# Performance work log

Measured on AMD Instinct MI355X. Metric: run time of the kernel, lower is better.

Reference implementation:

```python
import jax, jax.numpy as jnp
import numpy as np

FG_FRACTION = 0.5
BATCHSIZE = 256
NUM_IMAGES = 1
NUM_CLASSES = 21
FG_THRESH = 0.5
BG_THRESH_HI = 0.5
BG_THRESH_LO = 0.1
ROIS_PER_IMAGE = BATCHSIZE // NUM_IMAGES                      # 256
FG_ROIS_PER_IMAGE = int(round(FG_FRACTION * ROIS_PER_IMAGE))  # 128
BG_ROIS_PER_IMAGE = ROIS_PER_IMAGE - FG_ROIS_PER_IMAGE        # 128


def _make_boxes(key, n, img=1000.0, max_wh=200.0):
    k1, k2 = jax.random.split(key)
    xy = jax.random.uniform(k1, (n, 2), dtype=jnp.float32) * (img - max_wh)
    wh = jax.random.uniform(k2, (n, 2), dtype=jnp.float32) * max_wh + 1.0
    return jnp.concatenate([xy, xy + wh], axis=1)  # valid [x1,y1,x2,y2]


def setup_inputs() -> dict:
    key = jax.random.key(0)
    k1, k2, k3 = jax.random.split(key, 3)
    N, G = 250000, 128
    rois = _make_boxes(k1, N)
    all_rois = jnp.concatenate([jnp.zeros((N, 1), jnp.float32), rois], axis=1)  # [N,5], col0 = image idx
    gt_boxes = _make_boxes(k2, G)                                               # [G,4]
    gt_labels = jax.random.randint(k3, (G,), 1, NUM_CLASSES).astype(jnp.int32)  # fg classes 1..20
    return {"all_rois": all_rois, "gt_boxes": gt_boxes, "gt_labels": gt_labels}


def _iou(a, b):
    area_a = (a[:, 2] - a[:, 0] + 1.0) * (a[:, 3] - a[:, 1] + 1.0)
    area_b = (b[:, 2] - b[:, 0] + 1.0) * (b[:, 3] - b[:, 1] + 1.0)
    ix1 = jnp.maximum(a[:, None, 0], b[None, :, 0])
    iy1 = jnp.maximum(a[:, None, 1], b[None, :, 1])
    ix2 = jnp.minimum(a[:, None, 2], b[None, :, 2])
    iy2 = jnp.minimum(a[:, None, 3], b[None, :, 3])
    iw = jnp.clip(ix2 - ix1 + 1.0, 0.0)
    ih = jnp.clip(iy2 - iy1 + 1.0, 0.0)
    inter = iw * ih
    return inter / (area_a[:, None] + area_b[None, :] - inter)


def _bbox_transform(ex, gt):
    ew = ex[:, 2] - ex[:, 0] + 1.0
    eh = ex[:, 3] - ex[:, 1] + 1.0
    ecx = ex[:, 0] + 0.5 * ew
    ecy = ex[:, 1] + 0.5 * eh
    gw = gt[:, 2] - gt[:, 0] + 1.0
    gh = gt[:, 3] - gt[:, 1] + 1.0
    gcx = gt[:, 0] + 0.5 * gw
    gcy = gt[:, 1] + 0.5 * gh
    return jnp.stack([(gcx - ecx) / ew, (gcy - ecy) / eh,
                      jnp.log(gw / ew), jnp.log(gh / eh)], axis=1)


def _proposal_target(all_rois, gt_boxes, gt_labels):
    G = gt_boxes.shape[0]
    # append gt boxes (with image-index 0 column) to the proposal set
    gt_rois = jnp.concatenate([jnp.zeros((G, 1), all_rois.dtype), gt_boxes], axis=1)
    all_rois = jnp.concatenate([all_rois, gt_rois], axis=0)          # [N+G, 5]

    overlaps = _iou(all_rois[:, 1:5], gt_boxes)                       # [N+G, G] -- dominant memory traffic
    gt_assignment = jnp.argmax(overlaps, axis=1)                      # [N+G]
    max_ov = jnp.max(overlaps, axis=1)                                # [N+G]
    labels_all = gt_labels[gt_assignment]                             # [N+G]

    fg_mask = max_ov >= FG_THRESH
    bg_mask = (max_ov < BG_THRESH_HI) & (max_ov >= BG_THRESH_LO)

    # random fg/bg sampling: top-k over random keys restricted to each mask
    u = jax.random.uniform(jax.random.key(42), (all_rois.shape[0],), dtype=jnp.float32)
    fg_idx = jax.lax.top_k(jnp.where(fg_mask, u, -1.0), FG_ROIS_PER_IMAGE)[1]
    bg_idx = jax.lax.top_k(jnp.where(bg_mask, u, -1.0), BG_ROIS_PER_IMAGE)[1]
    keep = jnp.concatenate([fg_idx, bg_idx])                          # [256]

    valid_fg = fg_mask[fg_idx]  # if fewer fg than requested, pad slots get label 0
    labels = jnp.concatenate([jnp.where(valid_fg, labels_all[fg_idx], 0),
                              jnp.zeros((BG_ROIS_PER_IMAGE,), labels_all.dtype)])

    rois = all_rois[keep]                                             # [256, 5]
    targets = _bbox_transform(rois[:, 1:5], gt_boxes[gt_assignment[keep]])  # [256, 4]

    # scatter targets into class-specific columns [256, 4*num_classes]
    onehot = jax.nn.one_hot(labels, NUM_CLASSES, dtype=targets.dtype)
    bbox_targets = (onehot[:, :, None] * targets[:, None, :]).reshape(ROIS_PER_IMAGE, 4 * NUM_CLASSES)
    bbox_targets = bbox_targets * (labels > 0)[:, None].astype(targets.dtype)
    return rois, labels, bbox_targets


def reference(all_rois, gt_boxes, gt_labels):
    return _proposal_target(all_rois, gt_boxes, gt_labels)
```

## Files before the change

### kernel.cpp

```cpp
#include <hip/hip_runtime.h>
#include <stdint.h>

#define GMAX 128
#define TK 128
#define NBINS 4096
#define CAND_MAX 4096
#define NUM_CLASSES 21

__device__ __forceinline__ void threefry2x32(uint32_t k0, uint32_t k1,
                                             uint32_t& x0, uint32_t& x1) {
  uint32_t ks0 = k0, ks1 = k1, ks2 = k0 ^ k1 ^ 0x1BD11BDAu;
  x0 += ks0; x1 += ks1;
#define TF_ROUND(r) { x0 += x1; x1 = (x1 << (r)) | (x1 >> (32 - (r))); x1 ^= x0; }
  TF_ROUND(13) TF_ROUND(15) TF_ROUND(26) TF_ROUND(6)
  x0 += ks1; x1 += ks2 + 1u;
  TF_ROUND(17) TF_ROUND(29) TF_ROUND(16) TF_ROUND(24)
  x0 += ks2; x1 += ks0 + 2u;
  TF_ROUND(13) TF_ROUND(15) TF_ROUND(26) TF_ROUND(6)
  x0 += ks0; x1 += ks1 + 3u;
  TF_ROUND(17) TF_ROUND(29) TF_ROUND(16) TF_ROUND(24)
  x0 += ks1; x1 += ks2 + 4u;
  TF_ROUND(13) TF_ROUND(15) TF_ROUND(26) TF_ROUND(6)
  x0 += ks2; x1 += ks0 + 5u;
#undef TF_ROUND
}

__global__ void __launch_bounds__(1024)
init_kernel(uint32_t* __restrict__ hist, int* __restrict__ meta) {
  int i = blockIdx.x * 1024 + threadIdx.x;
  if (i < 2 * NBINS) hist[i] = 0u;
  if (i < 4) meta[i] = 0;
}

__global__ void __launch_bounds__(256)
score_kernel(const float* __restrict__ all_rois,
             const float* __restrict__ gt_boxes,
             uint32_t* __restrict__ score,
             uint32_t* __restrict__ hist,
             int N, int M, int G) {
  __shared__ float sgx1[GMAX], sgy1[GMAX], sgx2[GMAX], sgy2[GMAX], sga[GMAX];
  const int t = threadIdx.x;
  if (t < G) {
    float x1 = gt_boxes[t * 4 + 0];
    float y1 = gt_boxes[t * 4 + 1];
    float x2 = gt_boxes[t * 4 + 2];
    float y2 = gt_boxes[t * 4 + 3];
    sgx1[t] = x1; sgy1[t] = y1; sgx2[t] = x2; sgy2[t] = y2;
    sga[t] = __fmul_rn(__fadd_rn(__fsub_rn(x2, x1), 1.0f),
                       __fadd_rn(__fsub_rn(y2, y1), 1.0f));
  }
  __syncthreads();
  const int i = blockIdx.x * 256 + t;
  if (i >= M) return;

  float bx1, by1, bx2, by2;
  if (i < N) {
    bx1 = all_rois[(size_t)i * 5 + 1];
    by1 = all_rois[(size_t)i * 5 + 2];
    bx2 = all_rois[(size_t)i * 5 + 3];
    by2 = all_rois[(size_t)i * 5 + 4];
  } else {
    int g = i - N;
    bx1 = sgx1[g]; by1 = sgy1[g]; bx2 = sgx2[g]; by2 = sgy2[g];
  }
  const float area = __fmul_rn(__fadd_rn(__fsub_rn(bx2, bx1), 1.0f),
                               __fadd_rn(__fsub_rn(by2, by1), 1.0f));
  float best = -1.0f;
  int bi = 0;
  for (int g = 0; g < G; ++g) {
    float ix1 = fmaxf(bx1, sgx1[g]);
    float iy1 = fmaxf(by1, sgy1[g]);
    float ix2 = fminf(bx2, sgx2[g]);
    float iy2 = fminf(by2, sgy2[g]);
    float iw = fmaxf(__fadd_rn(__fsub_rn(ix2, ix1), 1.0f), 0.0f);
    float ih = fmaxf(__fadd_rn(__fsub_rn(iy2, iy1), 1.0f), 0.0f);
    float inter = __fmul_rn(iw, ih);
    float uni = __fsub_rn(__fadd_rn(area, sga[g]), inter);
    float ov = __fdiv_rn(inter, uni);
    if (ov > best) { best = ov; bi = g; }
  }

  uint32_t cx0 = 0u, cx1 = (uint32_t)i;
  threefry2x32(0u, 42u, cx0, cx1);
  uint32_t ubits = (cx0 ^ cx1) >> 9;

  uint32_t fg = (best >= 0.5f) ? 1u : 0u;
  uint32_t bg = (!fg && best >= 0.1f) ? 1u : 0u;
  score[i] = (ubits << 9) | ((uint32_t)bi << 2) | (fg << 1) | bg;
  if (fg)      atomicAdd(&hist[ubits >> 11], 1u);
  else if (bg) atomicAdd(&hist[NBINS + (ubits >> 11)], 1u);
}

__global__ void __launch_bounds__(1024)
threshold_kernel(const uint32_t* __restrict__ hist, int* __restrict__ meta) {
  __shared__ uint32_t gs[1024];
  __shared__ int s_jstar;
  const int t = threadIdx.x;
  for (int m = 0; m < 2; ++m) {
    const uint32_t* h = hist + m * NBINS;
    if (t == 0) s_jstar = -1;
    __syncthreads();
    gs[t] = h[4 * t] + h[4 * t + 1] + h[4 * t + 2] + h[4 * t + 3];
    __syncthreads();
    for (int d = 1; d < 1024; d <<= 1) {
      uint32_t add = (t + d < 1024) ? gs[t + d] : 0u;
      __syncthreads();
      gs[t] += add;
      __syncthreads();
    }
    if (gs[t] >= (uint32_t)TK && (t == 1023 || gs[t + 1] < (uint32_t)TK))
      s_jstar = t;
    __syncthreads();
    if (t == 0) {
      int B = -1;
      if (s_jstar >= 0) {
        int j = s_jstar;
        uint32_t base = (j < 1023) ? gs[j + 1] : 0u;
        B = 4 * j;
        for (int b = 4 * j + 3; b >= 4 * j; --b) {
          base += h[b];
          if (base >= (uint32_t)TK) { B = b; break; }
        }
      }
      meta[m] = B;
    }
    __syncthreads();
  }
}

__global__ void __launch_bounds__(1024)
compact_kernel(const uint32_t* __restrict__ score, int M,
               const int* __restrict__ meta_bth, int* __restrict__ meta_cnt,
               uint64_t* __restrict__ cand) {
  const int i = blockIdx.x * 1024 + threadIdx.x;
  if (i >= M) return;
  uint32_t s = score[i];
  uint32_t mb = s & 3u;
  if (!mb) return;
  const int m = (mb & 2u) ? 0 : 1;
  const int Bth = meta_bth[m];
  if (Bth >= 0 && (int)(s >> 20) < Bth) return;
  int p = atomicAdd(&meta_cnt[m], 1);
  if (p < CAND_MAX)
    cand[(size_t)m * CAND_MAX + p] =
        (((uint64_t)((s >> 9) + 1u)) << 32) | (uint64_t)(~(uint32_t)i);
}

__global__ void __launch_bounds__(1024)
final_kernel(const float* __restrict__ all_rois,
             const float* __restrict__ gt_boxes,
             const int* __restrict__ gt_labels,
             const uint32_t* __restrict__ score,
             const uint64_t* __restrict__ cand_g,
             const int* __restrict__ meta,
             float* __restrict__ out, int N, int M) {
  __shared__ uint64_t cand[CAND_MAX];
  __shared__ int keep[2 * TK];
  __shared__ int fgvalid[TK];
  __shared__ float s_tx[2 * TK], s_ty[2 * TK], s_tw[2 * TK], s_th[2 * TK];
  __shared__ int s_label[2 * TK];
  const int t = threadIdx.x;

  for (int m = 0; m < 2; ++m) {
    int cnt = meta[2 + m]; if (cnt > CAND_MAX) cnt = CAND_MAX;
    const int Bth = meta[m];
    int P = TK;
    while (P < cnt) P <<= 1;
    for (int p = t; p < P; p += 1024)
      cand[p] = (p < cnt) ? cand_g[(size_t)m * CAND_MAX + p] : 0ull;
    __syncthreads();
    for (int k = 2; k <= P; k <<= 1) {
      for (int j = k >> 1; j > 0; j >>= 1) {
        for (int idx = t; idx < P; idx += 1024) {
          int l = idx ^ j;
          if (l > idx) {
            uint64_t a = cand[idx], b = cand[l];
            bool swp = ((idx & k) == 0) ? (a < b) : (a > b);
            if (swp) { cand[idx] = b; cand[l] = a; }
          }
        }
        __syncthreads();
      }
    }
    if (Bth < 0 && t == 0) {
      int fill = cnt;
      uint32_t mask_bit = (m == 0) ? 2u : 1u;
      for (int i = 0; i < M && fill < TK; ++i)
        if (!(score[i] & mask_bit)) cand[fill++] = (uint64_t)(~(uint32_t)i);
    }
    __syncthreads();
    if (t < TK) {
      uint64_t c = cand[t];
      keep[m * TK + t] = (int)(~(uint32_t)(c & 0xFFFFFFFFull));
      if (m == 0) fgvalid[t] = ((c >> 32) != 0ull) ? 1 : 0;
    }
    __syncthreads();
  }

  const int R = 2 * TK;
  float* rois_out   = out;
  float* labels_out = out + (size_t)R * 5;
  float* bt_out     = out + (size_t)R * 5 + R;

  if (t < R) {
    const int i = keep[t];
    float rimg, rx1, ry1, rx2, ry2;
    if (i < N) {
      rimg = all_rois[(size_t)i * 5 + 0];
      rx1  = all_rois[(size_t)i * 5 + 1];
      ry1  = all_rois[(size_t)i * 5 + 2];
      rx2  = all_rois[(size_t)i * 5 + 3];
      ry2  = all_rois[(size_t)i * 5 + 4];
    } else {
      int g = i - N;
      rimg = 0.0f;
      rx1 = gt_boxes[g * 4 + 0]; ry1 = gt_boxes[g * 4 + 1];
      rx2 = gt_boxes[g * 4 + 2]; ry2 = gt_boxes[g * 4 + 3];
    }
    rois_out[t * 5 + 0] = rimg;
    rois_out[t * 5 + 1] = rx1;
    rois_out[t * 5 + 2] = ry1;
    rois_out[t * 5 + 3] = rx2;
    rois_out[t * 5 + 4] = ry2;

    const int ga = (int)((score[i] >> 2) & 127u);
    int label = (t < TK && fgvalid[t]) ? gt_labels[ga] : 0;
    labels_out[t] = (float)label;
    s_label[t] = label;

    float gx1 = gt_boxes[ga * 4 + 0], gy1 = gt_boxes[ga * 4 + 1];
    float gx2 = gt_boxes[ga * 4 + 2], gy2 = gt_boxes[ga * 4 + 3];
    float ew = rx2 - rx1 + 1.0f, eh = ry2 - ry1 + 1.0f;
    float ecx = rx1 + 0.5f * ew, ecy = ry1 + 0.5f * eh;
    float gw = gx2 - gx1 + 1.0f, gh = gy2 - gy1 + 1.0f;
    float gcx = gx1 + 0.5f * gw, gcy = gy1 + 0.5f * gh;
    s_tx[t] = (gcx - ecx) / ew;
    s_ty[t] = (gcy - ecy) / eh;
    s_tw[t] = logf(gw / ew);
    s_th[t] = logf(gh / eh);
  }
  __syncthreads();

  const int TOT = R * 4 * NUM_CLASSES;
  for (int idx = t; idx < TOT; idx += 1024) {
    int r = idx / (4 * NUM_CLASSES);
    int c = idx - r * (4 * NUM_CLASSES);
    int lab = s_label[r];
    float v = 0.0f;
    if (lab > 0 && (c >> 2) == lab) {
      int cc = c & 3;
      v = (cc == 0) ? s_tx[r] : (cc == 1) ? s_ty[r] : (cc == 2) ? s_tw[r] : s_th[r];
    }
    bt_out[idx] = v;
  }
}

extern "C" void kernel_launch(void* const* d_in, const int* in_sizes, int n_in,
                              void* d_out, int out_size, void* d_ws, size_t ws_size,
                              hipStream_t stream) {
  const float* all_rois = (const float*)d_in[0];
  const float* gt_boxes = (const float*)d_in[1];
  const int*   gt_labels = (const int*)d_in[2];
  const int N = in_sizes[0] / 5;
  const int G = in_sizes[2];
  const int M = N + G;

  char* ws = (char*)d_ws;
  uint32_t* score = (uint32_t*)ws;
  size_t off = (((size_t)M * 4) + 255) & ~(size_t)255;
  uint32_t* hist = (uint32_t*)(ws + off);  off += 2 * NBINS * 4;
  int* meta = (int*)(ws + off);            off += 256;
  uint64_t* cand = (uint64_t*)(ws + off);  off += 2 * (size_t)CAND_MAX * 8;
  float* out = (float*)d_out;

  init_kernel<<<(2 * NBINS + 1023) / 1024, 1024, 0, stream>>>(hist, meta);
  score_kernel<<<(M + 255) / 256, 256, 0, stream>>>(all_rois, gt_boxes, score,
                                                    hist, N, M, G);
  threshold_kernel<<<1, 1024, 0, stream>>>(hist, meta);
  compact_kernel<<<(M + 1023) / 1024, 1024, 0, stream>>>(score, M, meta,
                                                         meta + 2, cand);
  final_kernel<<<1, 1024, 0, stream>>>(all_rois, gt_boxes, gt_labels, score,
                                       cand, meta, out, N, M);
}
```

Measured before the change: 120.3 us.

## Fuse pipeline into one persistent kernel with software grid barriers

Replaces the five separate launches (init, score, threshold, compact, final) with a memset plus one persistent 256x1024 kernel that moves between phases using atomic-counter grid barriers. Scores stay in registers between the scoring and compaction phases, and every block computes the histogram threshold redundantly with a combined 64-bit fg/bg prefix scan. The aim is to remove launch overhead and the serial single-block threshold launch. In exchange, correctness depends on all 256 blocks being co-resident, and the scoring loop now runs on fewer threads with up to 8 items each.

```diff
diff --git a/kernel.cpp b/kernel.cpp
--- a/kernel.cpp
+++ b/kernel.cpp
@@ -6,6 +6,9 @@
 #define NBINS 4096
 #define CAND_MAX 4096
 #define NUM_CLASSES 21
+#define GRID 256
+#define BLOCK 1024
+#define EPT_MAX 8
 
 __device__ __forceinline__ void threefry2x32(uint32_t k0, uint32_t k1,
                                              uint32_t& x0, uint32_t& x1) {
@@ -25,21 +28,40 @@
 #undef TF_ROUND
 }
 
-__global__ void __launch_bounds__(1024)
-init_kernel(uint32_t* __restrict__ hist, int* __restrict__ meta) {
-  int i = blockIdx.x * 1024 + threadIdx.x;
-  if (i < 2 * NBINS) hist[i] = 0u;
-  if (i < 4) meta[i] = 0;
-}
-
-__global__ void __launch_bounds__(256)
-score_kernel(const float* __restrict__ all_rois,
+__device__ __forceinline__ void grid_barrier(int* ctr, int target) {
+  __threadfence();
+  __syncthreads();
+  if (threadIdx.x == 0) {
+    __hip_atomic_fetch_add(ctr, 1, __ATOMIC_ACQ_REL, __HIP_MEMORY_SCOPE_AGENT);
+    while (__hip_atomic_load(ctr, __ATOMIC_ACQUIRE, __HIP_MEMORY_SCOPE_AGENT) < target) {
+      __builtin_amdgcn_s_sleep(8);
+    }
+  }
+  __syncthreads();
+}
+
+__global__ void __launch_bounds__(BLOCK)
+fused_kernel(const float* __restrict__ all_rois,
              const float* __restrict__ gt_boxes,
+             const int* __restrict__ gt_labels,
+             int* __restrict__ meta,
+             uint32_t* __restrict__ hist,
              uint32_t* __restrict__ score,
-             uint32_t* __restrict__ hist,
+             uint64_t* __restrict__ cand_g,
+             float* __restrict__ out,
              int N, int M, int G) {
   __shared__ float sgx1[GMAX], sgy1[GMAX], sgx2[GMAX], sgy2[GMAX], sga[GMAX];
+  __shared__ uint64_t gs[BLOCK];
+  __shared__ int s_jstar[2], s_bth[2];
+  __shared__ uint64_t cand[CAND_MAX];
+  __shared__ int keep[2 * TK];
+  __shared__ int fgvalid[TK];
+  __shared__ float s_tx[2 * TK], s_ty[2 * TK], s_tw[2 * TK], s_th[2 * TK];
+  __shared__ int s_label[2 * TK];
+
   const int t = threadIdx.x;
+  const int stride = GRID * BLOCK;
+
   if (t < G) {
     float x1 = gt_boxes[t * 4 + 0];
     float y1 = gt_boxes[t * 4 + 1];
@@ -50,128 +72,120 @@
                        __fadd_rn(__fsub_rn(y2, y1), 1.0f));
   }
   __syncthreads();
-  const int i = blockIdx.x * 256 + t;
-  if (i >= M) return;
-
-  float bx1, by1, bx2, by2;
-  if (i < N) {
-    bx1 = all_rois[(size_t)i * 5 + 1];
-    by1 = all_rois[(size_t)i * 5 + 2];
-    bx2 = all_rois[(size_t)i * 5 + 3];
-    by2 = all_rois[(size_t)i * 5 + 4];
-  } else {
-    int g = i - N;
-    bx1 = sgx1[g]; by1 = sgy1[g]; bx2 = sgx2[g]; by2 = sgy2[g];
-  }
-  const float area = __fmul_rn(__fadd_rn(__fsub_rn(bx2, bx1), 1.0f),
-                               __fadd_rn(__fsub_rn(by2, by1), 1.0f));
-  float best = -1.0f;
-  int bi = 0;
-  for (int g = 0; g < G; ++g) {
-    float ix1 = fmaxf(bx1, sgx1[g]);
-    float iy1 = fmaxf(by1, sgy1[g]);
-    float ix2 = fminf(bx2, sgx2[g]);
-    float iy2 = fminf(by2, sgy2[g]);
-    float iw = fmaxf(__fadd_rn(__fsub_rn(ix2, ix1), 1.0f), 0.0f);
-    float ih = fmaxf(__fadd_rn(__fsub_rn(iy2, iy1), 1.0f), 0.0f);
-    float inter = __fmul_rn(iw, ih);
-    float uni = __fsub_rn(__fadd_rn(area, sga[g]), inter);
-    float ov = __fdiv_rn(inter, uni);
-    if (ov > best) { best = ov; bi = g; }
-  }
-
-  uint32_t cx0 = 0u, cx1 = (uint32_t)i;
-  threefry2x32(0u, 42u, cx0, cx1);
-  uint32_t ubits = (cx0 ^ cx1) >> 9;
-
-  uint32_t fg = (best >= 0.5f) ? 1u : 0u;
-  uint32_t bg = (!fg && best >= 0.1f) ? 1u : 0u;
-  score[i] = (ubits << 9) | ((uint32_t)bi << 2) | (fg << 1) | bg;
-  if (fg)      atomicAdd(&hist[ubits >> 11], 1u);
-  else if (bg) atomicAdd(&hist[NBINS + (ubits >> 11)], 1u);
-}
-
-__global__ void __launch_bounds__(1024)
-threshold_kernel(const uint32_t* __restrict__ hist, int* __restrict__ meta) {
-  __shared__ uint32_t gs[1024];
-  __shared__ int s_jstar;
-  const int t = threadIdx.x;
-  for (int m = 0; m < 2; ++m) {
-    const uint32_t* h = hist + m * NBINS;
-    if (t == 0) s_jstar = -1;
-    __syncthreads();
-    gs[t] = h[4 * t] + h[4 * t + 1] + h[4 * t + 2] + h[4 * t + 3];
-    __syncthreads();
-    for (int d = 1; d < 1024; d <<= 1) {
-      uint32_t add = (t + d < 1024) ? gs[t + d] : 0u;
+
+  uint32_t sv[EPT_MAX];
+  for (int i = blockIdx.x * BLOCK + t, e = 0; i < M && e < EPT_MAX;
+       i += stride, ++e) {
+    float bx1, by1, bx2, by2;
+    if (i < N) {
+      bx1 = all_rois[(size_t)i * 5 + 1];
+      by1 = all_rois[(size_t)i * 5 + 2];
+      bx2 = all_rois[(size_t)i * 5 + 3];
+      by2 = all_rois[(size_t)i * 5 + 4];
+    } else {
+      int g = i - N;
+      bx1 = sgx1[g]; by1 = sgy1[g]; bx2 = sgx2[g]; by2 = sgy2[g];
+    }
+    const float area = __fmul_rn(__fadd_rn(__fsub_rn(bx2, bx1), 1.0f),
+                                 __fadd_rn(__fsub_rn(by2, by1), 1.0f));
+    float best = -1.0f;
+    int bi = 0;
+    for (int g = 0; g < G; ++g) {
+      float ix1 = fmaxf(bx1, sgx1[g]);
+      float iy1 = fmaxf(by1, sgy1[g]);
+      float ix2 = fminf(bx2, sgx2[g]);
+      float iy2 = fminf(by2, sgy2[g]);
+      float iw = fmaxf(__fadd_rn(__fsub_rn(ix2, ix1), 1.0f), 0.0f);
+      float ih = fmaxf(__fadd_rn(__fsub_rn(iy2, iy1), 1.0f), 0.0f);
+      float inter = __fmul_rn(iw, ih);
+      float uni = __fsub_rn(__fadd_rn(area, sga[g]), inter);
+      float ov = __fdiv_rn(inter, uni);
+      if (ov > best) { best = ov; bi = g; }
+    }
+    uint32_t cx0 = 0u, cx1 = (uint32_t)i;
+    threefry2x32(0u, 42u, cx0, cx1);
+    uint32_t ubits = (cx0 ^ cx1) >> 9;
+    uint32_t fg = (best >= 0.5f) ? 1u : 0u;
+    uint32_t bg = (!fg && best >= 0.1f) ? 1u : 0u;
+    uint32_t s = (ubits << 9) | ((uint32_t)bi << 2) | (fg << 1) | bg;
+    sv[e] = s;
+    score[i] = s;
+    if (fg)      atomicAdd(&hist[ubits >> 11], 1u);
+    else if (bg) atomicAdd(&hist[NBINS + (ubits >> 11)], 1u);
+  }
+
+  grid_barrier(&meta[2], GRID);
+
+  {
+    const int b0 = 4 * t;
+    uint64_t acc = 0;
+    for (int k = 0; k < 4; ++k)
+      acc += ((uint64_t)hist[b0 + k] << 32) | (uint64_t)hist[NBINS + b0 + k];
+    gs[t] = acc;
+    if (t < 2) s_jstar[t] = -1;
+    __syncthreads();
+    for (int d = 1; d < BLOCK; d <<= 1) {
+      uint64_t add = (t + d < BLOCK) ? gs[t + d] : 0ull;
       __syncthreads();
       gs[t] += add;
       __syncthreads();
     }
-    if (gs[t] >= (uint32_t)TK && (t == 1023 || gs[t + 1] < (uint32_t)TK))
-      s_jstar = t;
+    uint32_t vfg = (uint32_t)(gs[t] >> 32);
+    uint32_t vbg = (uint32_t)gs[t];
+    uint32_t nfg = (t < BLOCK - 1) ? (uint32_t)(gs[t + 1] >> 32) : 0u;
+    uint32_t nbg = (t < BLOCK - 1) ? (uint32_t)gs[t + 1] : 0u;
+    if (vfg >= (uint32_t)TK && (t == BLOCK - 1 || nfg < (uint32_t)TK)) s_jstar[0] = t;
+    if (vbg >= (uint32_t)TK && (t == BLOCK - 1 || nbg < (uint32_t)TK)) s_jstar[1] = t;
     __syncthreads();
     if (t == 0) {
-      int B = -1;
-      if (s_jstar >= 0) {
-        int j = s_jstar;
-        uint32_t base = (j < 1023) ? gs[j + 1] : 0u;
-        B = 4 * j;
-        for (int b = 4 * j + 3; b >= 4 * j; --b) {
-          base += h[b];
-          if (base >= (uint32_t)TK) { B = b; break; }
+      for (int m = 0; m < 2; ++m) {
+        int j = s_jstar[m], B = -1;
+        if (j >= 0) {
+          uint32_t base = 0;
+          if (j < BLOCK - 1)
+            base = (m == 0) ? (uint32_t)(gs[j + 1] >> 32) : (uint32_t)gs[j + 1];
+          const uint32_t* h = hist + m * NBINS;
+          B = 4 * j;
+          for (int b = 4 * j + 3; b >= 4 * j; --b) {
+            base += h[b];
+            if (base >= (uint32_t)TK) { B = b; break; }
+          }
         }
+        s_bth[m] = B;
       }
-      meta[m] = B;
-    }
-    __syncthreads();
-  }
-}
-
-__global__ void __launch_bounds__(1024)
-compact_kernel(const uint32_t* __restrict__ score, int M,
-               const int* __restrict__ meta_bth, int* __restrict__ meta_cnt,
-               uint64_t* __restrict__ cand) {
-  const int i = blockIdx.x * 1024 + threadIdx.x;
-  if (i >= M) return;
-  uint32_t s = score[i];
-  uint32_t mb = s & 3u;
-  if (!mb) return;
-  const int m = (mb & 2u) ? 0 : 1;
-  const int Bth = meta_bth[m];
-  if (Bth >= 0 && (int)(s >> 20) < Bth) return;
-  int p = atomicAdd(&meta_cnt[m], 1);
-  if (p < CAND_MAX)
-    cand[(size_t)m * CAND_MAX + p] =
-        (((uint64_t)((s >> 9) + 1u)) << 32) | (uint64_t)(~(uint32_t)i);
-}
-
-__global__ void __launch_bounds__(1024)
-final_kernel(const float* __restrict__ all_rois,
-             const float* __restrict__ gt_boxes,
-             const int* __restrict__ gt_labels,
-             const uint32_t* __restrict__ score,
-             const uint64_t* __restrict__ cand_g,
-             const int* __restrict__ meta,
-             float* __restrict__ out, int N, int M) {
-  __shared__ uint64_t cand[CAND_MAX];
-  __shared__ int keep[2 * TK];
-  __shared__ int fgvalid[TK];
-  __shared__ float s_tx[2 * TK], s_ty[2 * TK], s_tw[2 * TK], s_th[2 * TK];
-  __shared__ int s_label[2 * TK];
-  const int t = threadIdx.x;
+    }
+    __syncthreads();
+  }
+
+  for (int i = blockIdx.x * BLOCK + t, e = 0; i < M && e < EPT_MAX;
+       i += stride, ++e) {
+    uint32_t s = sv[e];
+    uint32_t mb = s & 3u;
+    if (!mb) continue;
+    int m = (mb & 2u) ? 0 : 1;
+    int B = s_bth[m];
+    if (B >= 0 && (int)(s >> 20) < B) continue;
+    int p = __hip_atomic_fetch_add(&meta[m], 1, __ATOMIC_RELAXED,
+                                   __HIP_MEMORY_SCOPE_AGENT);
+    if (p < CAND_MAX)
+      cand_g[(size_t)m * CAND_MAX + p] =
+          (((uint64_t)((s >> 9) + 1u)) << 32) | (uint64_t)(~(uint32_t)i);
+  }
+
+  grid_barrier(&meta[2], 2 * GRID);
+  if (blockIdx.x != 0) return;
 
   for (int m = 0; m < 2; ++m) {
-    int cnt = meta[2 + m]; if (cnt > CAND_MAX) cnt = CAND_MAX;
-    const int Bth = meta[m];
+    int cnt = meta[m]; if (cnt > CAND_MAX) cnt = CAND_MAX;
+    const int Bth = s_bth[m];
     int P = TK;
     while (P < cnt) P <<= 1;
-    for (int p = t; p < P; p += 1024)
+    for (int p = t; p < P; p += BLOCK)
       cand[p] = (p < cnt) ? cand_g[(size_t)m * CAND_MAX + p] : 0ull;
     __syncthreads();
     for (int k = 2; k <= P; k <<= 1) {
       for (int j = k >> 1; j > 0; j >>= 1) {
-        for (int idx = t; idx < P; idx += 1024) {
+        for (int idx = t; idx < P; idx += BLOCK) {
           int l = idx ^ j;
           if (l > idx) {
             uint64_t a = cand[idx], b = cand[l];
@@ -242,7 +256,7 @@
   __syncthreads();
 
   const int TOT = R * 4 * NUM_CLASSES;
-  for (int idx = t; idx < TOT; idx += 1024) {
+  for (int idx = t; idx < TOT; idx += BLOCK) {
     int r = idx / (4 * NUM_CLASSES);
     int c = idx - r * (4 * NUM_CLASSES);
     int lab = s_label[r];
@@ -266,19 +280,16 @@
   const int M = N + G;
 
   char* ws = (char*)d_ws;
-  uint32_t* score = (uint32_t*)ws;
-  size_t off = (((size_t)M * 4) + 255) & ~(size_t)255;
-  uint32_t* hist = (uint32_t*)(ws + off);  off += 2 * NBINS * 4;
-  int* meta = (int*)(ws + off);            off += 256;
-  uint64_t* cand = (uint64_t*)(ws + off);  off += 2 * (size_t)CAND_MAX * 8;
+  int* meta = (int*)ws;
+  uint32_t* hist = (uint32_t*)(ws + 256);
+  size_t off = 256 + (size_t)2 * NBINS * 4;
+  uint32_t* score = (uint32_t*)(ws + off);
+  off += (((size_t)M * 4) + 255) & ~(size_t)255;
+  uint64_t* cand = (uint64_t*)(ws + off);
   float* out = (float*)d_out;
 
-  init_kernel<<<(2 * NBINS + 1023) / 1024, 1024, 0, stream>>>(hist, meta);
-  score_kernel<<<(M + 255) / 256, 256, 0, stream>>>(all_rois, gt_boxes, score,
-                                                    hist, N, M, G);
-  threshold_kernel<<<1, 1024, 0, stream>>>(hist, meta);
-  compact_kernel<<<(M + 1023) / 1024, 1024, 0, stream>>>(score, M, meta,
-                                                         meta + 2, cand);
-  final_kernel<<<1, 1024, 0, stream>>>(all_rois, gt_boxes, gt_labels, score,
-                                       cand, meta, out, N, M);
-}
+  hipMemsetAsync(ws, 0, 256 + (size_t)2 * NBINS * 4, stream);
+  fused_kernel<<<GRID, BLOCK, 0, stream>>>(all_rois, gt_boxes, gt_labels,
+                                           meta, hist, score, cand, out,
+                                           N, M, G);
+}
```

New measurement: 248.9 us. 107% more time.

## Fuse threshold scan into compact kernel and replace init kernel with memset

Applied to the files above, without the earlier changes.

Removes the single-block threshold kernel. Every compact block now redundantly prefix-scans both histograms at once, packing the fg and bg counts into one 64-bit value, and then filters scores with a grid-stride loop over a fixed 62 blocks. The init kernel becomes a hipMemsetAsync, and the fill-path condition now checks cnt < TK instead of a negative threshold. This drops one kernel launch and a serial dependency, at the cost of redundant per-block scans and fewer blocks for the compaction pass.

```diff
diff --git a/kernel.cpp b/kernel.cpp
--- a/kernel.cpp
+++ b/kernel.cpp
@@ -6,6 +6,8 @@
 #define NBINS 4096
 #define CAND_MAX 4096
 #define NUM_CLASSES 21
+#define CBLOCK 1024
+#define CBLOCKS 62
 
 __device__ __forceinline__ void threefry2x32(uint32_t k0, uint32_t k1,
                                              uint32_t& x0, uint32_t& x1) {
@@ -25,13 +27,6 @@
 #undef TF_ROUND
 }
 
-__global__ void __launch_bounds__(1024)
-init_kernel(uint32_t* __restrict__ hist, int* __restrict__ meta) {
-  int i = blockIdx.x * 1024 + threadIdx.x;
-  if (i < 2 * NBINS) hist[i] = 0u;
-  if (i < 4) meta[i] = 0;
-}
-
 __global__ void __launch_bounds__(256)
 score_kernel(const float* __restrict__ all_rois,
              const float* __restrict__ gt_boxes,
@@ -91,59 +86,68 @@
   else if (bg) atomicAdd(&hist[NBINS + (ubits >> 11)], 1u);
 }
 
-__global__ void __launch_bounds__(1024)
-threshold_kernel(const uint32_t* __restrict__ hist, int* __restrict__ meta) {
-  __shared__ uint32_t gs[1024];
-  __shared__ int s_jstar;
+__global__ void __launch_bounds__(CBLOCK)
+compact_kernel(const uint32_t* __restrict__ score, int M,
+               const uint32_t* __restrict__ hist,
+               int* __restrict__ meta_cnt,
+               uint64_t* __restrict__ cand) {
+  __shared__ uint64_t gs[CBLOCK];
+  __shared__ int s_jstar[2], s_bth[2];
   const int t = threadIdx.x;
-  for (int m = 0; m < 2; ++m) {
-    const uint32_t* h = hist + m * NBINS;
-    if (t == 0) s_jstar = -1;
-    __syncthreads();
-    gs[t] = h[4 * t] + h[4 * t + 1] + h[4 * t + 2] + h[4 * t + 3];
-    __syncthreads();
-    for (int d = 1; d < 1024; d <<= 1) {
-      uint32_t add = (t + d < 1024) ? gs[t + d] : 0u;
+
+  {
+    const int b0 = 4 * t;
+    uint64_t acc = 0;
+    for (int k = 0; k < 4; ++k)
+      acc += ((uint64_t)hist[b0 + k] << 32) | (uint64_t)hist[NBINS + b0 + k];
+    gs[t] = acc;
+    if (t < 2) s_jstar[t] = -1;
+    __syncthreads();
+    for (int d = 1; d < CBLOCK; d <<= 1) {
+      uint64_t add = (t + d < CBLOCK) ? gs[t + d] : 0ull;
       __syncthreads();
       gs[t] += add;
       __syncthreads();
     }
-    if (gs[t] >= (uint32_t)TK && (t == 1023 || gs[t + 1] < (uint32_t)TK))
-      s_jstar = t;
+    uint32_t vfg = (uint32_t)(gs[t] >> 32);
+    uint32_t vbg = (uint32_t)gs[t];
+    uint32_t nfg = (t < CBLOCK - 1) ? (uint32_t)(gs[t + 1] >> 32) : 0u;
+    uint32_t nbg = (t < CBLOCK - 1) ? (uint32_t)gs[t + 1] : 0u;
+    if (vfg >= (uint32_t)TK && (t == CBLOCK - 1 || nfg < (uint32_t)TK)) s_jstar[0] = t;
+    if (vbg >= (uint32_t)TK && (t == CBLOCK - 1 || nbg < (uint32_t)TK)) s_jstar[1] = t;
     __syncthreads();
     if (t == 0) {
-      int B = -1;
-      if (s_jstar >= 0) {
-        int j = s_jstar;
-        uint32_t base = (j < 1023) ? gs[j + 1] : 0u;
-        B = 4 * j;
-        for (int b = 4 * j + 3; b >= 4 * j; --b) {
-          base += h[b];
-          if (base >= (uint32_t)TK) { B = b; break; }
+      for (int m = 0; m < 2; ++m) {
+        int j = s_jstar[m], B = -1;
+        if (j >= 0) {
+          uint32_t base = 0;
+          if (j < CBLOCK - 1)
+            base = (m == 0) ? (uint32_t)(gs[j + 1] >> 32) : (uint32_t)gs[j + 1];
+          const uint32_t* h = hist + m * NBINS;
+          B = 4 * j;
+          for (int b = 4 * j + 3; b >= 4 * j; --b) {
+            base += h[b];
+            if (base >= (uint32_t)TK) { B = b; break; }
+          }
         }
+        s_bth[m] = B;
       }
-      meta[m] = B;
-    }
-    __syncthreads();
-  }
-}
-
-__global__ void __launch_bounds__(1024)
-compact_kernel(const uint32_t* __restrict__ score, int M,
-               const int* __restrict__ meta_bth, int* __restrict__ meta_cnt,
-               uint64_t* __restrict__ cand) {
-  const int i = blockIdx.x * 1024 + threadIdx.x;
-  if (i >= M) return;
-  uint32_t s = score[i];
-  uint32_t mb = s & 3u;
-  if (!mb) return;
-  const int m = (mb & 2u) ? 0 : 1;
-  const int Bth = meta_bth[m];
-  if (Bth >= 0 && (int)(s >> 20) < Bth) return;
-  int p = atomicAdd(&meta_cnt[m], 1);
-  if (p < CAND_MAX)
-    cand[(size_t)m * CAND_MAX + p] =
-        (((uint64_t)((s >> 9) + 1u)) << 32) | (uint64_t)(~(uint32_t)i);
+    }
+    __syncthreads();
+  }
+
+  for (int i = blockIdx.x * CBLOCK + t; i < M; i += CBLOCKS * CBLOCK) {
+    uint32_t s = score[i];
+    uint32_t mb = s & 3u;
+    if (!mb) continue;
+    int m = (mb & 2u) ? 0 : 1;
+    int B = s_bth[m];
+    if (B >= 0 && (int)(s >> 20) < B) continue;
+    int p = atomicAdd(&meta_cnt[m], 1);
+    if (p < CAND_MAX)
+      cand[(size_t)m * CAND_MAX + p] =
+          (((uint64_t)((s >> 9) + 1u)) << 32) | (uint64_t)(~(uint32_t)i);
+  }
 }
 
 __global__ void __launch_bounds__(1024)
@@ -152,7 +156,7 @@
              const int* __restrict__ gt_labels,
              const uint32_t* __restrict__ score,
              const uint64_t* __restrict__ cand_g,
-             const int* __restrict__ meta,
+             const int* __restrict__ meta_cnt,
              float* __restrict__ out, int N, int M) {
   __shared__ uint64_t cand[CAND_MAX];
   __shared__ int keep[2 * TK];
@@ -162,8 +166,7 @@
   const int t = threadIdx.x;
 
   for (int m = 0; m < 2; ++m) {
-    int cnt = meta[2 + m]; if (cnt > CAND_MAX) cnt = CAND_MAX;
-    const int Bth = meta[m];
+    int cnt = meta_cnt[m]; if (cnt > CAND_MAX) cnt = CAND_MAX;
     int P = TK;
     while (P < cnt) P <<= 1;
     for (int p = t; p < P; p += 1024)
@@ -182,7 +185,7 @@
         __syncthreads();
       }
     }
-    if (Bth < 0 && t == 0) {
+    if (cnt < TK && t == 0) {
       int fill = cnt;
       uint32_t mask_bit = (m == 0) ? 2u : 1u;
       for (int i = 0; i < M && fill < TK; ++i)
@@ -266,19 +269,18 @@
   const int M = N + G;
 
   char* ws = (char*)d_ws;
-  uint32_t* score = (uint32_t*)ws;
-  size_t off = (((size_t)M * 4) + 255) & ~(size_t)255;
-  uint32_t* hist = (uint32_t*)(ws + off);  off += 2 * NBINS * 4;
-  int* meta = (int*)(ws + off);            off += 256;
-  uint64_t* cand = (uint64_t*)(ws + off);  off += 2 * (size_t)CAND_MAX * 8;
+  int* meta = (int*)ws;
+  uint32_t* hist = (uint32_t*)(ws + 256);
+  size_t off = 256 + (size_t)2 * NBINS * 4;
+  uint32_t* score = (uint32_t*)(ws + off);
+  off += (((size_t)M * 4) + 255) & ~(size_t)255;
+  uint64_t* cand = (uint64_t*)(ws + off);
   float* out = (float*)d_out;
 
-  init_kernel<<<(2 * NBINS + 1023) / 1024, 1024, 0, stream>>>(hist, meta);
+  hipMemsetAsync(ws, 0, 256 + (size_t)2 * NBINS * 4, stream);
   score_kernel<<<(M + 255) / 256, 256, 0, stream>>>(all_rois, gt_boxes, score,
                                                     hist, N, M, G);
-  threshold_kernel<<<1, 1024, 0, stream>>>(hist, meta);
-  compact_kernel<<<(M + 1023) / 1024, 1024, 0, stream>>>(score, M, meta,
-                                                         meta + 2, cand);
+  compact_kernel<<<CBLOCKS, CBLOCK, 0, stream>>>(score, M, hist, meta, cand);
   final_kernel<<<1, 1024, 0, stream>>>(all_rois, gt_boxes, gt_labels, score,
                                        cand, meta, out, N, M);
 }
```

After: 116.8 us. 3.0% less time.
